# Performance work log

Measured on AMD Instinct MI355X. Metric: run time of the kernel, lower is better.

Reference implementation:

```python
import jax, jax.numpy as jnp
import numpy as np
from jax import lax

F_SIZE = 128
N_HEADS = 8
HEAD_D = F_SIZE // N_HEADS
LANE_F = 64
NUM_PREDS = 6


def _layernorm(x, g, b, eps=1e-5):
    m = x.mean(-1, keepdims=True)
    v = jnp.var(x, axis=-1, keepdims=True)
    return (x - m) * lax.rsqrt(v + eps) * g + b


def _lstm_cell(x, h, c, wih, whh, bih, bhh):
    # PyTorch LSTMCell: gates ordered i, f, g, o
    gates = x @ wih.T + bih + h @ whh.T + bhh
    i, f, g, o = jnp.split(gates, 4, axis=-1)
    c2 = jax.nn.sigmoid(f) * c + jax.nn.sigmoid(i) * jnp.tanh(g)
    h2 = jax.nn.sigmoid(o) * jnp.tanh(c2)
    return h2, c2


def _to_xy(dl, yaw):
    return jnp.concatenate([dl * jnp.cos(yaw), dl * jnp.sin(yaw)], axis=-1)


def _attention(tok_pos, h_ego, h, lane_tok, key_mask, wq, wk, wv, wo, pos_w, pos_b):
    # tokens = [ego, vehicles], keys/values = [tokens, lanes]
    B = h_ego.shape[0]
    tok = jnp.concatenate([h_ego, h], axis=1) + tok_pos @ pos_w + pos_b  # [B,N1,F]
    kv = jnp.concatenate([tok, lane_tok], axis=1)  # [B,N1+L,F]
    q = (tok @ wq).reshape(B, -1, N_HEADS, HEAD_D)
    k = (kv @ wk).reshape(B, -1, N_HEADS, HEAD_D)
    v = (kv @ wv).reshape(B, -1, N_HEADS, HEAD_D)
    s = jnp.einsum('bqhd,bkhd->bhqk', q, k) / jnp.asarray(np.sqrt(HEAD_D), jnp.float32)
    s = jnp.where(key_mask[:, None, None, :] > 0, s, -1e9)
    a = jax.nn.softmax(s, axis=-1)
    o = jnp.einsum('bhqk,bkhd->bqhd', a, v).reshape(B, -1, F_SIZE) @ wo
    tok = tok + o
    return tok[:, :1], tok[:, 1:]


def _forward(input, init_pos, lane_input, mask_input, lane_mask,
             conv_w, conv_b, pos_w, pos_b,
             lane_w1, lane_b1, lane_w2, lane_b2, lane_to_f,
             wq, wk, wv, wo, ln_ego_g, ln_ego_b, ln_g, ln_b,
             ego_wih, ego_whh, ego_bih, ego_bhh,
             veh_wih, veh_whh, veh_bih, veh_bhh,
             out_ego_w, out_ego_b, out_w, out_b, len_pred):
    T, B, N1, _ = input.shape
    V = N1 - 1
    Hh = T - 2  # valid conv over time with kernel 3

    # shared conv_input applied to ego+vehicles at once (same weights in original)
    x = jnp.transpose(input, (1, 3, 2, 0))  # [B,2,N1,T]
    feat = lax.conv_general_dilated(x, conv_w, (1, 1), 'VALID',
                                    dimension_numbers=('NCHW', 'OIHW', 'NCHW'))
    feat = feat + conv_b[None, :, None, None]
    feat = jnp.transpose(feat, (3, 0, 2, 1))  # [Hh,B,N1,F]
    h_ego_seq, h_seq = feat[:, :, :1], feat[:, :, 1:]

    # lane embedding: per-point MLP + mean pool
    lanes = jax.nn.relu(lane_input @ lane_w1 + lane_b1)
    lanes = jax.nn.relu(lanes @ lane_w2 + lane_b2).mean(axis=2)  # [B,L,LANE_F]
    lane_tok = lanes @ lane_to_f  # [B,L,F]
    key_mask = jnp.concatenate([mask_input, lane_mask], axis=1)  # [B,N1+L]

    pos0 = init_pos[0]
    pe0, pv0 = pos0[:, :1], pos0[:, 1:]

    def cell_step(hx_ego, cx_ego, hx, cx, he, hv, pe, pv):
        tok_pos = jnp.concatenate([pe, pv], axis=1)
        ae, av = _attention(tok_pos, he, hv, lane_tok, key_mask, wq, wk, wv, wo, pos_w, pos_b)
        ae = _layernorm(ae.reshape(B, F_SIZE), ln_ego_g, ln_ego_b)
        av = _layernorm(av.reshape(B * V, F_SIZE), ln_g, ln_b)
        hx_ego, cx_ego = _lstm_cell(ae, hx_ego, cx_ego, ego_wih, ego_whh, ego_bih, ego_bhh)
        hx, cx = _lstm_cell(av, hx, cx, veh_wih, veh_whh, veh_bih, veh_bhh)
        return hx_ego, cx_ego, hx, cx

    def hist_step(carry, xs):
        hx_ego, cx_ego, hx, cx, pe, pv = carry
        he, hv, xe, xv = xs
        pe = pe + _to_xy(xe[..., 0:1], xe[..., 1:2])
        pv = pv + _to_xy(xv[..., 0:1], xv[..., 1:2])
        hx_ego, cx_ego, hx, cx = cell_step(hx_ego, cx_ego, hx, cx, he, hv, pe, pv)
        return (hx_ego, cx_ego, hx, cx, pe, pv), None

    carry0 = (jnp.zeros((B, F_SIZE)), jnp.zeros((B, F_SIZE)),
              jnp.zeros((B * V, F_SIZE)), jnp.zeros((B * V, F_SIZE)), pe0, pv0)
    xs = (h_ego_seq, h_seq, input[:Hh, :, :1, :].transpose(0, 1, 2, 3), input[:Hh, :, 1:, :])
    carry, _ = lax.scan(hist_step, carry0, xs)
    hx_ego, cx_ego, hx, cx, pe, pv = carry

    pe = jnp.repeat(pe[:, :, None, :], NUM_PREDS, axis=2)  # [B,1,P,2]
    pv = jnp.repeat(pv[:, :, None, :], NUM_PREDS, axis=2)  # [B,V,P,2]

    def pred_step(carry, _):
        hx_ego, cx_ego, hx, cx, pe, pv = carry
        he = hx_ego.reshape(B, 1, F_SIZE)
        hv = hx.reshape(B, V, F_SIZE)
        hx_ego, cx_ego, hx, cx = cell_step(hx_ego, cx_ego, hx, cx, he, hv,
                                           pe.mean(axis=2), pv.mean(axis=2))
        oe = (hx_ego @ out_ego_w + out_ego_b).reshape(B, 1, NUM_PREDS, 6)
        ov = (hx @ out_w + out_b).reshape(B, V, NUM_PREDS, 6)
        pe = pe + _to_xy(oe[..., 0:1], oe[..., 1:2])
        pv = pv + _to_xy(ov[..., 0:1], ov[..., 1:2])
        y = jnp.concatenate([
            jnp.concatenate([pe, oe[..., 2:6]], axis=-1),
            jnp.concatenate([pv, ov[..., 2:6]], axis=-1)], axis=1)  # [B,N1,P,6]
        return (hx_ego, cx_ego, hx, cx, pe, pv), y

    carry = (hx_ego, cx_ego, hx, cx, pe, pv)
    _, ys = lax.scan(pred_step, carry, None, length=len_pred)
    return ys  # [len_pred,B,N1,NUM_PREDS,6]


def setup_inputs() -> dict:
    key = jax.random.key(0)
    ks = jax.random.split(key, 40)
    B, T, N1, L, PTS = 128, 22, 32, 64, 10
    F, LF, G4, P6 = F_SIZE, LANE_F, 4 * F_SIZE, NUM_PREDS * 6
    s = 0.05
    inp = {}
    inp['input'] = jax.random.normal(ks[0], (T, B, N1, 2), jnp.float32) * 0.1
    inp['init_pos'] = jax.random.normal(ks[1], (1, B, N1, 2), jnp.float32) * 10.0
    inp['lane_input'] = jax.random.normal(ks[2], (B, L, PTS, 2), jnp.float32)
    inp['mask_input'] = jnp.ones((B, N1), jnp.float32)
    inp['lane_mask'] = jnp.ones((B, L), jnp.float32)
    inp['conv_w'] = jax.random.normal(ks[3], (F, 2, 1, 3), jnp.float32) * s
    inp['conv_b'] = jnp.zeros((F,), jnp.float32)
    inp['pos_w'] = jax.random.normal(ks[4], (2, F), jnp.float32) * s
    inp['pos_b'] = jnp.zeros((F,), jnp.float32)
    inp['lane_w1'] = jax.random.normal(ks[5], (2, LF), jnp.float32) * s
    inp['lane_b1'] = jnp.zeros((LF,), jnp.float32)
    inp['lane_w2'] = jax.random.normal(ks[6], (LF, LF), jnp.float32) * s
    inp['lane_b2'] = jnp.zeros((LF,), jnp.float32)
    inp['lane_to_f'] = jax.random.normal(ks[7], (LF, F), jnp.float32) * s
    inp['wq'] = jax.random.normal(ks[8], (F, F), jnp.float32) * s
    inp['wk'] = jax.random.normal(ks[9], (F, F), jnp.float32) * s
    inp['wv'] = jax.random.normal(ks[10], (F, F), jnp.float32) * s
    inp['wo'] = jax.random.normal(ks[11], (F, F), jnp.float32) * s
    inp['ln_ego_g'] = jnp.ones((F,), jnp.float32)
    inp['ln_ego_b'] = jnp.zeros((F,), jnp.float32)
    inp['ln_g'] = jnp.ones((F,), jnp.float32)
    inp['ln_b'] = jnp.zeros((F,), jnp.float32)
    inp['ego_wih'] = jax.random.normal(ks[12], (G4, F), jnp.float32) * s
    inp['ego_whh'] = jax.random.normal(ks[13], (G4, F), jnp.float32) * s
    inp['ego_bih'] = jnp.zeros((G4,), jnp.float32)
    inp['ego_bhh'] = jnp.zeros((G4,), jnp.float32)
    inp['veh_wih'] = jax.random.normal(ks[14], (G4, F), jnp.float32) * s
    inp['veh_whh'] = jax.random.normal(ks[15], (G4, F), jnp.float32) * s
    inp['veh_bih'] = jnp.zeros((G4,), jnp.float32)
    inp['veh_bhh'] = jnp.zeros((G4,), jnp.float32)
    inp['out_ego_w'] = jax.random.normal(ks[16], (F, P6), jnp.float32) * s
    inp['out_ego_b'] = jnp.zeros((P6,), jnp.float32)
    inp['out_w'] = jax.random.normal(ks[17], (F, P6), jnp.float32) * s
    inp['out_b'] = jnp.zeros((P6,), jnp.float32)
    inp['len_pred'] = 30
    return inp


def reference(input, init_pos, lane_input, mask_input, lane_mask,
              conv_w, conv_b, pos_w, pos_b,
              lane_w1, lane_b1, lane_w2, lane_b2, lane_to_f,
              wq, wk, wv, wo, ln_ego_g, ln_ego_b, ln_g, ln_b,
              ego_wih, ego_whh, ego_bih, ego_bhh,
              veh_wih, veh_whh, veh_bih, veh_bhh,
              out_ego_w, out_ego_b, out_w, out_b, len_pred):
    return _forward(input, init_pos, lane_input, mask_input, lane_mask,
                    conv_w, conv_b, pos_w, pos_b,
                    lane_w1, lane_b1, lane_w2, lane_b2, lane_to_f,
                    wq, wk, wv, wo, ln_ego_g, ln_ego_b, ln_g, ln_b,
                    ego_wih, ego_whh, ego_bih, ego_bhh,
                    veh_wih, veh_whh, veh_bih, veh_bhh,
                    out_ego_w, out_ego_b, out_w, out_b, len_pred)
```

## Files before the change

### kernel.cpp

```cpp
#include <hip/hip_runtime.h>
#include <hip/hip_bf16.h>
#include <math.h>

constexpr int B   = 128;
constexpr int T   = 22;
constexpr int N1  = 32;
constexpr int HH  = 20;
constexpr int L   = 64;
constexpr int PTS = 10;
constexpr int F   = 128;
constexpr int LF  = 64;
constexpr int NH  = 8;
constexpr int HD  = 16;
constexpr int KVN = 96;
constexpr int G4  = 512;
constexpr int NP  = 6;
constexpr int P6  = 36;
constexpr int LEN = 30;

__device__ __forceinline__ float sigmoidf(float x) { return 1.f / (1.f + expf(-x)); }


__global__ void k_lane_tok(const float* __restrict__ lane_input,
                           const float* __restrict__ w1, const float* __restrict__ b1,
                           const float* __restrict__ w2, const float* __restrict__ b2,
                           const float* __restrict__ to_f,
                           float* __restrict__ kvbuf) {
    int bl = blockIdx.x; int b = bl / L, l = bl % L;
    int tid = threadIdx.x;
    __shared__ float h1[PTS][LF];
    __shared__ float m[LF];
    const float* xin = lane_input + ((size_t)(b * L + l) * PTS) * 2;
    float w10 = w1[tid], w11 = w1[LF + tid], bb1 = b1[tid];
    for (int p = 0; p < PTS; ++p) {
        float v = xin[p * 2] * w10 + xin[p * 2 + 1] * w11 + bb1;
        h1[p][tid] = fmaxf(v, 0.f);
    }
    __syncthreads();
    float acc = 0.f;
    for (int p = 0; p < PTS; ++p) {
        float s = b2[tid];
        for (int h = 0; h < LF; ++h) s += h1[p][h] * w2[h * LF + tid];
        acc += fmaxf(s, 0.f);
    }
    m[tid] = acc * (1.f / PTS);
    __syncthreads();
    float* out = kvbuf + ((size_t)(b * KVN) + 32 + l) * F;
    for (int f = tid; f < F; f += LF) {
        float s = 0.f;
        for (int j = 0; j < LF; ++j) s += m[j] * to_f[j * F + f];
        out[f] = s;
    }
}

__global__ void k_hist_pos(const float* __restrict__ input,
                           const float* __restrict__ init_pos,
                           float* __restrict__ hist_pos) {
    int idx = blockIdx.x * blockDim.x + threadIdx.x;
    if (idx >= B * N1) return;
    float px = init_pos[idx * 2], py = init_pos[idx * 2 + 1];
    int b = idx / N1, n = idx % N1;
    for (int t = 0; t < HH; ++t) {
        const float* ip = input + ((size_t)(t * B + b) * N1 + n) * 2;
        float dl = ip[0], yaw = ip[1];
        px += dl * cosf(yaw);
        py += dl * sinf(yaw);
        float* hp = hist_pos + ((size_t)(t * B + b) * N1 + n) * 2;
        hp[0] = px; hp[1] = py;
    }
}

__global__ void k_transpose_w(const float* __restrict__ w, float* __restrict__ wt) {
    int i = blockIdx.x * blockDim.x + threadIdx.x;
    if (i >= G4 * F) return;
    int j = i / F, k2 = i % F;
    wt[k2 * G4 + j] = w[i];
}

__global__ void k_init_predpos(const float* __restrict__ hist_pos, float* __restrict__ pred_pos) {
    int i = blockIdx.x * blockDim.x + threadIdx.x;
    if (i >= B * N1 * NP * 2) return;
    int c = i & 1;
    int bn = i / (2 * NP);
    pred_pos[i] = hist_pos[((size_t)(HH - 1) * B * N1 + bn) * 2 + c];
}


__global__ void k_tok_hist(const float* __restrict__ input,
                           const float* __restrict__ conv_w, const float* __restrict__ conv_b,
                           const float* __restrict__ pos_w, const float* __restrict__ pos_b,
                           const float* __restrict__ hist_pos,
                           float* __restrict__ kvbuf, int t) {
    int bn = blockIdx.x; int b = bn / N1, n = bn % N1;
    int f = threadIdx.x;
    float acc = conv_b[f];
#pragma unroll
    for (int kt = 0; kt < 3; ++kt) {
        const float* ip = input + ((size_t)((t + kt) * B + b) * N1 + n) * 2;
        acc += ip[0] * conv_w[(f * 2 + 0) * 3 + kt] + ip[1] * conv_w[(f * 2 + 1) * 3 + kt];
    }
    const float* hp = hist_pos + ((size_t)(t * B + b) * N1 + n) * 2;
    acc += hp[0] * pos_w[f] + hp[1] * pos_w[F + f] + pos_b[f];
    kvbuf[((size_t)b * KVN + n) * F + f] = acc;
}

__global__ void k_tok_pred(const float* __restrict__ h, const float* __restrict__ pred_pos,
                           const float* __restrict__ pos_w, const float* __restrict__ pos_b,
                           float* __restrict__ kvbuf) {
    int bn = blockIdx.x; int b = bn / N1, n = bn % N1;
    int f = threadIdx.x;
    const float* pp = pred_pos + (size_t)bn * NP * 2;
    float mx = 0.f, my = 0.f;
#pragma unroll
    for (int p = 0; p < NP; ++p) { mx += pp[p * 2]; my += pp[p * 2 + 1]; }
    mx *= (1.f / NP); my *= (1.f / NP);
    float tok = h[(size_t)bn * F + f] + mx * pos_w[f] + my * pos_w[F + f] + pos_b[f];
    kvbuf[((size_t)b * KVN + n) * F + f] = tok;
}

__global__ void k_qkv(const float* __restrict__ kvbuf,
                      const float* __restrict__ wq, const float* __restrict__ wk,
                      const float* __restrict__ wv,
                      float* __restrict__ qbuf, float* __restrict__ kbuf,
                      float* __restrict__ vbuf) {
    int g = blockIdx.x % 28, b = blockIdx.x / 28;
    int j = threadIdx.x;
    const float* W; float* out; int row0;
    if (g < 4)       { W = wq; row0 = g * 8;        out = qbuf + ((size_t)b * N1  + row0) * F; }
    else if (g < 16) { W = wk; row0 = (g - 4) * 8;  out = kbuf + ((size_t)b * KVN + row0) * F; }
    else             { W = wv; row0 = (g - 16) * 8; out = vbuf + ((size_t)b * KVN + row0) * F; }
    const float* in = kvbuf + ((size_t)b * KVN + row0) * F;
    __shared__ float rows[8][F];
#pragma unroll
    for (int r = 0; r < 8; ++r) rows[r][j] = in[r * F + j];
    __syncthreads();
    float acc[8] = {0, 0, 0, 0, 0, 0, 0, 0};
    for (int k2 = 0; k2 < F; ++k2) {
        float w = W[k2 * F + j];
#pragma unroll
        for (int r = 0; r < 8; ++r) acc[r] += rows[r][k2] * w;
    }
#pragma unroll
    for (int r = 0; r < 8; ++r) out[r * F + j] = acc[r];
}

__global__ void k_attn(const float* __restrict__ qbuf, const float* __restrict__ kbuf,
                       const float* __restrict__ vbuf,
                       const float* __restrict__ mask_in, const float* __restrict__ lane_mask,
                       float* __restrict__ attno) {
    int h = blockIdx.x % NH, b = blockIdx.x / NH;
    int tid = threadIdx.x;
    __shared__ float qs[N1][HD];
    __shared__ float s[N1][KVN];
    for (int i = tid; i < N1 * HD; i += 128) {
        int qr = i / HD, d = i % HD;
        qs[qr][d] = qbuf[((size_t)b * N1 + qr) * F + h * HD + d];
    }
    __syncthreads();
    for (int i = tid; i < N1 * KVN; i += 128) {
        int qr = i / KVN, kc = i % KVN;
        const float* kp = kbuf + ((size_t)b * KVN + kc) * F + h * HD;
        float acc = 0.f;
#pragma unroll
        for (int d = 0; d < HD; ++d) acc += qs[qr][d] * kp[d];
        float mval = (kc < N1) ? mask_in[b * N1 + kc] : lane_mask[b * L + (kc - N1)];
        s[qr][kc] = (mval > 0.f) ? acc * 0.25f : -1e9f;
    }
    __syncthreads();
    if (tid < N1) {
        float mx = -1e30f;
        for (int kc = 0; kc < KVN; ++kc) mx = fmaxf(mx, s[tid][kc]);
        float sum = 0.f;
        for (int kc = 0; kc < KVN; ++kc) { float e = expf(s[tid][kc] - mx); s[tid][kc] = e; sum += e; }
        float inv = 1.f / sum;
        for (int kc = 0; kc < KVN; ++kc) s[tid][kc] *= inv;
    }
    __syncthreads();
    for (int i = tid; i < N1 * HD; i += 128) {
        int qr = i / HD, d = i % HD;
        float acc = 0.f;
        for (int kc = 0; kc < KVN; ++kc)
            acc += s[qr][kc] * vbuf[((size_t)b * KVN + kc) * F + h * HD + d];
        attno[((size_t)b * N1 + qr) * F + h * HD + d] = acc;
    }
}

__global__ void k_proj_ln(const float* __restrict__ attno, const float* __restrict__ kvbuf,
                          const float* __restrict__ wo,
                          const float* __restrict__ ln_ego_g, const float* __restrict__ ln_ego_b,
                          const float* __restrict__ ln_g, const float* __restrict__ ln_b,
                          float* __restrict__ xln) {
    int gi = blockIdx.x; int b = gi / 8, n0 = (gi % 8) * 4;
    int j = threadIdx.x;
    __shared__ float arows[4][F];
    __shared__ float p1[2], p2[2];
#pragma unroll
    for (int r = 0; r < 4; ++r) arows[r][j] = attno[((size_t)b * N1 + n0 + r) * F + j];
    __syncthreads();
    float acc[4] = {0, 0, 0, 0};
    for (int k2 = 0; k2 < F; ++k2) {
        float w = wo[k2 * F + j];
#pragma unroll
        for (int r = 0; r < 4; ++r) acc[r] += arows[r][k2] * w;
    }
    for (int r = 0; r < 4; ++r) {
        int n = n0 + r;
        float x = kvbuf[((size_t)b * KVN + n) * F + j] + acc[r];
        float s1 = x, s2 = x * x;
#pragma unroll
        for (int off = 32; off > 0; off >>= 1) {
            s1 += __shfl_down(s1, off, 64);
            s2 += __shfl_down(s2, off, 64);
        }
        if ((j & 63) == 0) { p1[j >> 6] = s1; p2[j >> 6] = s2; }
        __syncthreads();
        float mean = (p1[0] + p1[1]) * (1.f / F);
        float var  = (p2[0] + p2[1]) * (1.f / F) - mean * mean;
        float rstd = rsqrtf(var + 1e-5f);
        const float* g  = (n == 0) ? ln_ego_g : ln_g;
        const float* bb = (n == 0) ? ln_ego_b : ln_b;
        xln[((size_t)b * N1 + n) * F + j] = (x - mean) * rstd * g[j] + bb[j];
        __syncthreads();
    }
}

__global__ void k_lstm(const float* __restrict__ xln,
                       const float* __restrict__ ego_wih_t, const float* __restrict__ ego_whh_t,
                       const float* __restrict__ ego_bih, const float* __restrict__ ego_bhh,
                       const float* __restrict__ veh_wih_t, const float* __restrict__ veh_whh_t,
                       const float* __restrict__ veh_bih, const float* __restrict__ veh_bhh,
                       float* __restrict__ h, float* __restrict__ c) {
    int n = blockIdx.x / 16; int b0 = (blockIdx.x % 16) * 8;
    int j = threadIdx.x;
    const float *wih, *whh, *bih, *bhh;
    if (n == 0) { wih = ego_wih_t; whh = ego_whh_t; bih = ego_bih; bhh = ego_bhh; }
    else        { wih = veh_wih_t; whh = veh_whh_t; bih = veh_bih; bhh = veh_bhh; }
    __shared__ float xr[8][F], hr[8][F];
    __shared__ float gs[8][G4];
    for (int i = j; i < 8 * F; i += 512) {
        int r = i / F, k2 = i % F;
        size_t bn = (size_t)(b0 + r) * N1 + n;
        xr[r][k2] = xln[bn * F + k2];
        hr[r][k2] = h[bn * F + k2];
    }
    __syncthreads();
    float acc[8];
    float bsum = bih[j] + bhh[j];
#pragma unroll
    for (int r = 0; r < 8; ++r) acc[r] = bsum;
    for (int k2 = 0; k2 < F; ++k2) {
        float w1 = wih[k2 * G4 + j];
        float w2 = whh[k2 * G4 + j];
#pragma unroll
        for (int r = 0; r < 8; ++r) acc[r] += xr[r][k2] * w1 + hr[r][k2] * w2;
    }
#pragma unroll
    for (int r = 0; r < 8; ++r) gs[r][j] = acc[r];
    __syncthreads();
    for (int i = j; i < 8 * F; i += 512) {
        int r = i / F, f = i % F;
        size_t bn = (size_t)(b0 + r) * N1 + n;
        float ig = gs[r][f], fg = gs[r][F + f], gg = gs[r][2 * F + f], og = gs[r][3 * F + f];
        float cold = c[bn * F + f];
        float c2 = sigmoidf(fg) * cold + sigmoidf(ig) * tanhf(gg);
        float h2 = sigmoidf(og) * tanhf(c2);
        c[bn * F + f] = c2;
        h[bn * F + f] = h2;
    }
}

__global__ void k_pred_out(const float* __restrict__ h,
                           const float* __restrict__ out_ego_w, const float* __restrict__ out_ego_b,
                           const float* __restrict__ out_w, const float* __restrict__ out_b,
                           float* __restrict__ pred_pos, float* __restrict__ out, int step) {
    int bn = blockIdx.x; int n = bn % N1;
    int j = threadIdx.x;
    __shared__ float hrow[F];
    __shared__ float o36[P6];
    hrow[j] = h[(size_t)bn * F + j];
    hrow[j + 64] = h[(size_t)bn * F + j + 64];
    __syncthreads();
    const float* W  = (n == 0) ? out_ego_w : out_w;
    const float* bb = (n == 0) ? out_ego_b : out_b;
    if (j < P6) {
        float acc = bb[j];
        for (int k2 = 0; k2 < F; ++k2) acc += hrow[k2] * W[k2 * P6 + j];
        o36[j] = acc;
    }
    __syncthreads();
    if (j < NP) {
        float dl = o36[j * 6], yaw = o36[j * 6 + 1];
        float* pp = pred_pos + ((size_t)bn * NP + j) * 2;
        float px = pp[0] + dl * cosf(yaw);
        float py = pp[1] + dl * sinf(yaw);
        pp[0] = px; pp[1] = py;
        float* y = out + (size_t)step * B * N1 * P6 + ((size_t)bn * NP + j) * 6;
        y[0] = px; y[1] = py;
        y[2] = o36[j * 6 + 2]; y[3] = o36[j * 6 + 3];
        y[4] = o36[j * 6 + 4]; y[5] = o36[j * 6 + 5];
    }
}

extern "C" void kernel_launch(void* const* d_in, const int* in_sizes, int n_in,
                              void* d_out, int out_size, void* d_ws, size_t ws_size,
                              hipStream_t stream) {
    const float* input      = (const float*)d_in[0];
    const float* init_pos   = (const float*)d_in[1];
    const float* lane_input = (const float*)d_in[2];
    const float* mask_input = (const float*)d_in[3];
    const float* lane_mask  = (const float*)d_in[4];
    const float* conv_w     = (const float*)d_in[5];
    const float* conv_b     = (const float*)d_in[6];
    const float* pos_w      = (const float*)d_in[7];
    const float* pos_b      = (const float*)d_in[8];
    const float* lane_w1    = (const float*)d_in[9];
    const float* lane_b1    = (const float*)d_in[10];
    const float* lane_w2    = (const float*)d_in[11];
    const float* lane_b2    = (const float*)d_in[12];
    const float* lane_to_f  = (const float*)d_in[13];
    const float* wq         = (const float*)d_in[14];
    const float* wk         = (const float*)d_in[15];
    const float* wv         = (const float*)d_in[16];
    const float* wo         = (const float*)d_in[17];
    const float* ln_ego_g   = (const float*)d_in[18];
    const float* ln_ego_b   = (const float*)d_in[19];
    const float* ln_g       = (const float*)d_in[20];
    const float* ln_b       = (const float*)d_in[21];
    const float* ego_wih    = (const float*)d_in[22];
    const float* ego_whh    = (const float*)d_in[23];
    const float* ego_bih    = (const float*)d_in[24];
    const float* ego_bhh    = (const float*)d_in[25];
    const float* veh_wih    = (const float*)d_in[26];
    const float* veh_whh    = (const float*)d_in[27];
    const float* veh_bih    = (const float*)d_in[28];
    const float* veh_bhh    = (const float*)d_in[29];
    const float* out_ego_w  = (const float*)d_in[30];
    const float* out_ego_b  = (const float*)d_in[31];
    const float* out_w      = (const float*)d_in[32];
    const float* out_b      = (const float*)d_in[33];

    float* out = (float*)d_out;
    float* ws = (float*)d_ws;

    float* kv       = ws;
    float* qb       = kv + (size_t)B * KVN * F;
    float* kb       = qb + (size_t)B * N1 * F;
    float* vb       = kb + (size_t)B * KVN * F;
    float* attno    = vb + (size_t)B * KVN * F;
    float* xln      = attno + (size_t)B * N1 * F;
    float* hbuf     = xln + (size_t)B * N1 * F;
    float* cbuf     = hbuf + (size_t)B * N1 * F;
    float* hist_pos = cbuf + (size_t)B * N1 * F;
    float* pred_pos = hist_pos + (size_t)HH * B * N1 * 2;
    float* wt       = pred_pos + (size_t)B * N1 * NP * 2;
    float* ego_wih_t = wt;
    float* ego_whh_t = wt + (size_t)G4 * F;
    float* veh_wih_t = wt + (size_t)2 * G4 * F;
    float* veh_whh_t = wt + (size_t)3 * G4 * F;

    hipMemsetAsync(hbuf, 0, (size_t)B * N1 * F * sizeof(float), stream);
    hipMemsetAsync(cbuf, 0, (size_t)B * N1 * F * sizeof(float), stream);
    k_lane_tok<<<B * L, 64, 0, stream>>>(lane_input, lane_w1, lane_b1, lane_w2, lane_b2,
                                         lane_to_f, kv);
    k_hist_pos<<<(B * N1 + 255) / 256, 256, 0, stream>>>(input, init_pos, hist_pos);
    k_transpose_w<<<(G4 * F + 255) / 256, 256, 0, stream>>>(ego_wih, ego_wih_t);
    k_transpose_w<<<(G4 * F + 255) / 256, 256, 0, stream>>>(ego_whh, ego_whh_t);
    k_transpose_w<<<(G4 * F + 255) / 256, 256, 0, stream>>>(veh_wih, veh_wih_t);
    k_transpose_w<<<(G4 * F + 255) / 256, 256, 0, stream>>>(veh_whh, veh_whh_t);

    for (int t = 0; t < HH; ++t) {
        k_tok_hist<<<B * N1, F, 0, stream>>>(input, conv_w, conv_b, pos_w, pos_b,
                                             hist_pos, kv, t);
        k_qkv<<<B * 28, F, 0, stream>>>(kv, wq, wk, wv, qb, kb, vb);
        k_attn<<<B * NH, 128, 0, stream>>>(qb, kb, vb, mask_input, lane_mask, attno);
        k_proj_ln<<<B * 8, 128, 0, stream>>>(attno, kv, wo, ln_ego_g, ln_ego_b, ln_g, ln_b, xln);
        k_lstm<<<N1 * 16, G4, 0, stream>>>(xln, ego_wih_t, ego_whh_t, ego_bih, ego_bhh,
                                           veh_wih_t, veh_whh_t, veh_bih, veh_bhh, hbuf, cbuf);
    }

    k_init_predpos<<<(B * N1 * NP * 2 + 255) / 256, 256, 0, stream>>>(hist_pos, pred_pos);

    for (int s = 0; s < LEN; ++s) {
        k_tok_pred<<<B * N1, F, 0, stream>>>(hbuf, pred_pos, pos_w, pos_b, kv);
        k_qkv<<<B * 28, F, 0, stream>>>(kv, wq, wk, wv, qb, kb, vb);
        k_attn<<<B * NH, 128, 0, stream>>>(qb, kb, vb, mask_input, lane_mask, attno);
        k_proj_ln<<<B * 8, 128, 0, stream>>>(attno, kv, wo, ln_ego_g, ln_ego_b, ln_g, ln_b, xln);
        k_lstm<<<N1 * 16, G4, 0, stream>>>(xln, ego_wih_t, ego_whh_t, ego_bih, ego_bhh,
                                           veh_wih_t, veh_whh_t, veh_bih, veh_bhh, hbuf, cbuf);
        k_pred_out<<<B * N1, 64, 0, stream>>>(hbuf, out_ego_w, out_ego_b, out_w, out_b,
                                              pred_pos, out, s);
    }
}
```

Baseline: 6.342 ms.

## Fuse per-step kernels and hoist loop-invariant lane K/V projection

Cuts the per-step kernel chain from five or six launches to three. Token building is fused with the Q/K/V projection, attention is fused with the output projection and LayerNorm (one block per batch), and the LSTM is fused with the prediction head. Lane K/V projections never change across steps, so they are computed once before the loops instead of every step. The trade-off is much less parallelism per launch: the attention kernel runs only 128 blocks and loops over heads serially, and the LSTM kernel runs 256 blocks with 16 rows each, which may underfill the GPU.

```diff
diff --git a/kernel.cpp b/kernel.cpp
--- a/kernel.cpp
+++ b/kernel.cpp
@@ -3,7 +3,6 @@
 #include <math.h>
 
 constexpr int B   = 128;
-constexpr int T   = 22;
 constexpr int N1  = 32;
 constexpr int HH  = 20;
 constexpr int L   = 64;
@@ -45,17 +44,49 @@
     }
     m[tid] = acc * (1.f / PTS);
     __syncthreads();
-    float* out = kvbuf + ((size_t)(b * KVN) + 32 + l) * F;
+    float* outp = kvbuf + ((size_t)(b * KVN) + 32 + l) * F;
     for (int f = tid; f < F; f += LF) {
         float s = 0.f;
         for (int j = 0; j < LF; ++j) s += m[j] * to_f[j * F + f];
-        out[f] = s;
+        outp[f] = s;
+    }
+}
+
+__global__ void k_lane_kv(const float* __restrict__ kvbuf,
+                          const float* __restrict__ wk, const float* __restrict__ wv,
+                          float* __restrict__ kb, float* __restrict__ vb) {
+    int g = blockIdx.x & 7, b = blockIdx.x >> 3;
+    int n0 = 32 + g * 8;
+    int tid = threadIdx.x;
+    int j = tid & 127, rh = tid >> 7;
+    __shared__ float tok[8][F];
+    for (int i = tid; i < 8 * F; i += 256) {
+        int r = i >> 7, c = i & 127;
+        tok[r][c] = kvbuf[((size_t)b * KVN + n0 + r) * F + c];
+    }
+    __syncthreads();
+    float ak[4] = {0, 0, 0, 0}, av[4] = {0, 0, 0, 0};
+    int r0 = rh * 4;
+    for (int k2 = 0; k2 < F; ++k2) {
+        float wkv = wk[k2 * F + j], wvv = wv[k2 * F + j];
+#pragma unroll
+        for (int r = 0; r < 4; ++r) {
+            float x = tok[r0 + r][k2];
+            ak[r] += x * wkv; av[r] += x * wvv;
+        }
+    }
+#pragma unroll
+    for (int r = 0; r < 4; ++r) {
+        int n = n0 + r0 + r;
+        kb[((size_t)b * KVN + n) * F + j] = ak[r];
+        vb[((size_t)b * KVN + n) * F + j] = av[r];
     }
 }
 
 __global__ void k_hist_pos(const float* __restrict__ input,
                            const float* __restrict__ init_pos,
-                           float* __restrict__ hist_pos) {
+                           float* __restrict__ hist_pos,
+                           float* __restrict__ pred_pos) {
     int idx = blockIdx.x * blockDim.x + threadIdx.x;
     if (idx >= B * N1) return;
     float px = init_pos[idx * 2], py = init_pos[idx * 2 + 1];
@@ -68,197 +99,209 @@
         float* hp = hist_pos + ((size_t)(t * B + b) * N1 + n) * 2;
         hp[0] = px; hp[1] = py;
     }
-}
-
-__global__ void k_transpose_w(const float* __restrict__ w, float* __restrict__ wt) {
+#pragma unroll
+    for (int p = 0; p < NP; ++p) {
+        pred_pos[((size_t)idx * NP + p) * 2 + 0] = px;
+        pred_pos[((size_t)idx * NP + p) * 2 + 1] = py;
+    }
+}
+
+__global__ void k_transpose_all(const float* __restrict__ w0, const float* __restrict__ w1,
+                                const float* __restrict__ w2, const float* __restrict__ w3,
+                                float* __restrict__ wt) {
     int i = blockIdx.x * blockDim.x + threadIdx.x;
-    if (i >= G4 * F) return;
-    int j = i / F, k2 = i % F;
-    wt[k2 * G4 + j] = w[i];
-}
-
-__global__ void k_init_predpos(const float* __restrict__ hist_pos, float* __restrict__ pred_pos) {
-    int i = blockIdx.x * blockDim.x + threadIdx.x;
-    if (i >= B * N1 * NP * 2) return;
-    int c = i & 1;
-    int bn = i / (2 * NP);
-    pred_pos[i] = hist_pos[((size_t)(HH - 1) * B * N1 + bn) * 2 + c];
-}
-
-
-__global__ void k_tok_hist(const float* __restrict__ input,
-                           const float* __restrict__ conv_w, const float* __restrict__ conv_b,
-                           const float* __restrict__ pos_w, const float* __restrict__ pos_b,
-                           const float* __restrict__ hist_pos,
-                           float* __restrict__ kvbuf, int t) {
-    int bn = blockIdx.x; int b = bn / N1, n = bn % N1;
-    int f = threadIdx.x;
-    float acc = conv_b[f];
-#pragma unroll
-    for (int kt = 0; kt < 3; ++kt) {
-        const float* ip = input + ((size_t)((t + kt) * B + b) * N1 + n) * 2;
-        acc += ip[0] * conv_w[(f * 2 + 0) * 3 + kt] + ip[1] * conv_w[(f * 2 + 1) * 3 + kt];
-    }
-    const float* hp = hist_pos + ((size_t)(t * B + b) * N1 + n) * 2;
-    acc += hp[0] * pos_w[f] + hp[1] * pos_w[F + f] + pos_b[f];
-    kvbuf[((size_t)b * KVN + n) * F + f] = acc;
-}
-
-__global__ void k_tok_pred(const float* __restrict__ h, const float* __restrict__ pred_pos,
-                           const float* __restrict__ pos_w, const float* __restrict__ pos_b,
-                           float* __restrict__ kvbuf) {
-    int bn = blockIdx.x; int b = bn / N1, n = bn % N1;
-    int f = threadIdx.x;
-    const float* pp = pred_pos + (size_t)bn * NP * 2;
-    float mx = 0.f, my = 0.f;
-#pragma unroll
-    for (int p = 0; p < NP; ++p) { mx += pp[p * 2]; my += pp[p * 2 + 1]; }
-    mx *= (1.f / NP); my *= (1.f / NP);
-    float tok = h[(size_t)bn * F + f] + mx * pos_w[f] + my * pos_w[F + f] + pos_b[f];
-    kvbuf[((size_t)b * KVN + n) * F + f] = tok;
-}
-
-__global__ void k_qkv(const float* __restrict__ kvbuf,
-                      const float* __restrict__ wq, const float* __restrict__ wk,
-                      const float* __restrict__ wv,
-                      float* __restrict__ qbuf, float* __restrict__ kbuf,
-                      float* __restrict__ vbuf) {
-    int g = blockIdx.x % 28, b = blockIdx.x / 28;
-    int j = threadIdx.x;
-    const float* W; float* out; int row0;
-    if (g < 4)       { W = wq; row0 = g * 8;        out = qbuf + ((size_t)b * N1  + row0) * F; }
-    else if (g < 16) { W = wk; row0 = (g - 4) * 8;  out = kbuf + ((size_t)b * KVN + row0) * F; }
-    else             { W = wv; row0 = (g - 16) * 8; out = vbuf + ((size_t)b * KVN + row0) * F; }
-    const float* in = kvbuf + ((size_t)b * KVN + row0) * F;
-    __shared__ float rows[8][F];
-#pragma unroll
-    for (int r = 0; r < 8; ++r) rows[r][j] = in[r * F + j];
-    __syncthreads();
+    if (i >= 4 * G4 * F) return;
+    int m = i / (G4 * F), rem = i % (G4 * F);
+    int j = rem / F, k2 = rem % F;
+    const float* src = (m == 0) ? w0 : (m == 1) ? w1 : (m == 2) ? w2 : w3;
+    wt[(size_t)m * G4 * F + (size_t)k2 * G4 + j] = src[rem];
+}
+
+
+__global__ void k_tok_qkv(const float* __restrict__ input, const float* __restrict__ hist_pos,
+                          const float* __restrict__ h, const float* __restrict__ pred_pos,
+                          const float* __restrict__ conv_w, const float* __restrict__ conv_b,
+                          const float* __restrict__ pos_w, const float* __restrict__ pos_b,
+                          const float* __restrict__ wq, const float* __restrict__ wk,
+                          const float* __restrict__ wv,
+                          float* __restrict__ kvbuf, float* __restrict__ qb,
+                          float* __restrict__ kb, float* __restrict__ vb,
+                          int mode, int t) {
+    int g = blockIdx.x & 3, b = blockIdx.x >> 2;
+    int n0 = g * 8;
+    int tid = threadIdx.x;
+    int j = tid & 127, rh = tid >> 7;
+    __shared__ float tok[8][F];
+    for (int i = tid; i < 8 * F; i += 256) {
+        int r = i >> 7, c = i & 127;
+        int n = n0 + r;
+        float acc;
+        if (mode == 0) {
+            acc = conv_b[c];
+#pragma unroll
+            for (int kt = 0; kt < 3; ++kt) {
+                const float* ip = input + ((size_t)((t + kt) * B + b) * N1 + n) * 2;
+                acc += ip[0] * conv_w[(c * 2 + 0) * 3 + kt] + ip[1] * conv_w[(c * 2 + 1) * 3 + kt];
+            }
+            const float* hp = hist_pos + ((size_t)(t * B + b) * N1 + n) * 2;
+            acc += hp[0] * pos_w[c] + hp[1] * pos_w[F + c] + pos_b[c];
+        } else {
+            const float* pp = pred_pos + ((size_t)(b * N1 + n)) * NP * 2;
+            float mx = 0.f, my = 0.f;
+#pragma unroll
+            for (int p = 0; p < NP; ++p) { mx += pp[p * 2]; my += pp[p * 2 + 1]; }
+            mx *= (1.f / NP); my *= (1.f / NP);
+            acc = h[((size_t)b * N1 + n) * F + c] + mx * pos_w[c] + my * pos_w[F + c] + pos_b[c];
+        }
+        tok[r][c] = acc;
+        kvbuf[((size_t)b * KVN + n) * F + c] = acc;
+    }
+    __syncthreads();
+    float aq[4] = {0, 0, 0, 0}, ak[4] = {0, 0, 0, 0}, av[4] = {0, 0, 0, 0};
+    int r0 = rh * 4;
+    for (int k2 = 0; k2 < F; ++k2) {
+        float wqv = wq[k2 * F + j], wkv = wk[k2 * F + j], wvv = wv[k2 * F + j];
+#pragma unroll
+        for (int r = 0; r < 4; ++r) {
+            float x = tok[r0 + r][k2];
+            aq[r] += x * wqv; ak[r] += x * wkv; av[r] += x * wvv;
+        }
+    }
+#pragma unroll
+    for (int r = 0; r < 4; ++r) {
+        int n = n0 + r0 + r;
+        qb[((size_t)b * N1 + n) * F + j]  = aq[r];
+        kb[((size_t)b * KVN + n) * F + j] = ak[r];
+        vb[((size_t)b * KVN + n) * F + j] = av[r];
+    }
+}
+
+__global__ void k_attn_proj_ln(const float* __restrict__ qb, const float* __restrict__ kb,
+                               const float* __restrict__ vb, const float* __restrict__ kvbuf,
+                               const float* __restrict__ mask_in, const float* __restrict__ lane_mask,
+                               const float* __restrict__ wo,
+                               const float* __restrict__ ln_ego_g, const float* __restrict__ ln_ego_b,
+                               const float* __restrict__ ln_g, const float* __restrict__ ln_b,
+                               float* __restrict__ xln) {
+    int b = blockIdx.x;
+    int tid = threadIdx.x;
+    __shared__ float qh[N1][HD];
+    __shared__ float kh[KVN][HD];
+    __shared__ float vh[KVN][HD];
+    __shared__ float sc[N1][KVN + 1];
+    __shared__ float ao[N1][F];
+    __shared__ float xb[N1][F];
+    __shared__ float red[N1][2];
+
+    for (int h = 0; h < NH; ++h) {
+        if (tid < N1 * HD) {
+            int qr = tid >> 4, d = tid & 15;
+            qh[qr][d] = qb[((size_t)b * N1 + qr) * F + h * HD + d];
+        }
+        for (int i = tid; i < KVN * HD; i += 512) {
+            int kc = i >> 4, d = i & 15;
+            kh[kc][d] = kb[((size_t)b * KVN + kc) * F + h * HD + d];
+            vh[kc][d] = vb[((size_t)b * KVN + kc) * F + h * HD + d];
+        }
+        __syncthreads();
+        for (int i = tid; i < N1 * KVN; i += 512) {
+            int qr = i / KVN, kc = i % KVN;
+            float acc = 0.f;
+#pragma unroll
+            for (int d = 0; d < HD; ++d) acc += qh[qr][d] * kh[kc][d];
+            float mval = (kc < N1) ? mask_in[b * N1 + kc] : lane_mask[b * L + (kc - N1)];
+            sc[qr][kc] = (mval > 0.f) ? acc * 0.25f : -1e9f;
+        }
+        __syncthreads();
+        if (tid < N1) {
+            float mx = -1e30f;
+            for (int kc = 0; kc < KVN; ++kc) mx = fmaxf(mx, sc[tid][kc]);
+            float sum = 0.f;
+            for (int kc = 0; kc < KVN; ++kc) { float e = expf(sc[tid][kc] - mx); sc[tid][kc] = e; sum += e; }
+            float inv = 1.f / sum;
+            for (int kc = 0; kc < KVN; ++kc) sc[tid][kc] *= inv;
+        }
+        __syncthreads();
+        if (tid < N1 * HD) {
+            int qr = tid >> 4, d = tid & 15;
+            float acc = 0.f;
+            for (int kc = 0; kc < KVN; ++kc) acc += sc[qr][kc] * vh[kc][d];
+            ao[qr][h * HD + d] = acc;
+        }
+        __syncthreads();
+    }
+    int j = tid & 127, rh = tid >> 7;
     float acc[8] = {0, 0, 0, 0, 0, 0, 0, 0};
-    for (int k2 = 0; k2 < F; ++k2) {
-        float w = W[k2 * F + j];
-#pragma unroll
-        for (int r = 0; r < 8; ++r) acc[r] += rows[r][k2] * w;
-    }
-#pragma unroll
-    for (int r = 0; r < 8; ++r) out[r * F + j] = acc[r];
-}
-
-__global__ void k_attn(const float* __restrict__ qbuf, const float* __restrict__ kbuf,
-                       const float* __restrict__ vbuf,
-                       const float* __restrict__ mask_in, const float* __restrict__ lane_mask,
-                       float* __restrict__ attno) {
-    int h = blockIdx.x % NH, b = blockIdx.x / NH;
-    int tid = threadIdx.x;
-    __shared__ float qs[N1][HD];
-    __shared__ float s[N1][KVN];
-    for (int i = tid; i < N1 * HD; i += 128) {
-        int qr = i / HD, d = i % HD;
-        qs[qr][d] = qbuf[((size_t)b * N1 + qr) * F + h * HD + d];
-    }
-    __syncthreads();
-    for (int i = tid; i < N1 * KVN; i += 128) {
-        int qr = i / KVN, kc = i % KVN;
-        const float* kp = kbuf + ((size_t)b * KVN + kc) * F + h * HD;
-        float acc = 0.f;
-#pragma unroll
-        for (int d = 0; d < HD; ++d) acc += qs[qr][d] * kp[d];
-        float mval = (kc < N1) ? mask_in[b * N1 + kc] : lane_mask[b * L + (kc - N1)];
-        s[qr][kc] = (mval > 0.f) ? acc * 0.25f : -1e9f;
-    }
-    __syncthreads();
-    if (tid < N1) {
-        float mx = -1e30f;
-        for (int kc = 0; kc < KVN; ++kc) mx = fmaxf(mx, s[tid][kc]);
-        float sum = 0.f;
-        for (int kc = 0; kc < KVN; ++kc) { float e = expf(s[tid][kc] - mx); s[tid][kc] = e; sum += e; }
-        float inv = 1.f / sum;
-        for (int kc = 0; kc < KVN; ++kc) s[tid][kc] *= inv;
-    }
-    __syncthreads();
-    for (int i = tid; i < N1 * HD; i += 128) {
-        int qr = i / HD, d = i % HD;
-        float acc = 0.f;
-        for (int kc = 0; kc < KVN; ++kc)
-            acc += s[qr][kc] * vbuf[((size_t)b * KVN + kc) * F + h * HD + d];
-        attno[((size_t)b * N1 + qr) * F + h * HD + d] = acc;
-    }
-}
-
-__global__ void k_proj_ln(const float* __restrict__ attno, const float* __restrict__ kvbuf,
-                          const float* __restrict__ wo,
-                          const float* __restrict__ ln_ego_g, const float* __restrict__ ln_ego_b,
-                          const float* __restrict__ ln_g, const float* __restrict__ ln_b,
-                          float* __restrict__ xln) {
-    int gi = blockIdx.x; int b = gi / 8, n0 = (gi % 8) * 4;
-    int j = threadIdx.x;
-    __shared__ float arows[4][F];
-    __shared__ float p1[2], p2[2];
-#pragma unroll
-    for (int r = 0; r < 4; ++r) arows[r][j] = attno[((size_t)b * N1 + n0 + r) * F + j];
-    __syncthreads();
-    float acc[4] = {0, 0, 0, 0};
+    int r0 = rh * 8;
     for (int k2 = 0; k2 < F; ++k2) {
         float w = wo[k2 * F + j];
 #pragma unroll
-        for (int r = 0; r < 4; ++r) acc[r] += arows[r][k2] * w;
-    }
-    for (int r = 0; r < 4; ++r) {
-        int n = n0 + r;
-        float x = kvbuf[((size_t)b * KVN + n) * F + j] + acc[r];
-        float s1 = x, s2 = x * x;
-#pragma unroll
-        for (int off = 32; off > 0; off >>= 1) {
-            s1 += __shfl_down(s1, off, 64);
-            s2 += __shfl_down(s2, off, 64);
-        }
-        if ((j & 63) == 0) { p1[j >> 6] = s1; p2[j >> 6] = s2; }
-        __syncthreads();
-        float mean = (p1[0] + p1[1]) * (1.f / F);
-        float var  = (p2[0] + p2[1]) * (1.f / F) - mean * mean;
-        float rstd = rsqrtf(var + 1e-5f);
-        const float* g  = (n == 0) ? ln_ego_g : ln_g;
-        const float* bb = (n == 0) ? ln_ego_b : ln_b;
-        xln[((size_t)b * N1 + n) * F + j] = (x - mean) * rstd * g[j] + bb[j];
-        __syncthreads();
-    }
-}
-
-__global__ void k_lstm(const float* __restrict__ xln,
-                       const float* __restrict__ ego_wih_t, const float* __restrict__ ego_whh_t,
-                       const float* __restrict__ ego_bih, const float* __restrict__ ego_bhh,
-                       const float* __restrict__ veh_wih_t, const float* __restrict__ veh_whh_t,
-                       const float* __restrict__ veh_bih, const float* __restrict__ veh_bhh,
-                       float* __restrict__ h, float* __restrict__ c) {
-    int n = blockIdx.x / 16; int b0 = (blockIdx.x % 16) * 8;
+        for (int r = 0; r < 8; ++r) acc[r] += ao[r0 + r][k2] * w;
+    }
+#pragma unroll
+    for (int r = 0; r < 8; ++r) {
+        int n = r0 + r;
+        xb[n][j] = kvbuf[((size_t)b * KVN + n) * F + j] + acc[r];
+    }
+    __syncthreads();
+    if (tid < N1) {
+        float s1 = 0.f, s2 = 0.f;
+        for (int c = 0; c < F; ++c) { float x = xb[tid][c]; s1 += x; s2 += x * x; }
+        float mean = s1 * (1.f / F);
+        float var = s2 * (1.f / F) - mean * mean;
+        red[tid][0] = mean;
+        red[tid][1] = rsqrtf(var + 1e-5f);
+    }
+    __syncthreads();
+    for (int i = tid; i < N1 * F; i += 512) {
+        int r = i >> 7, c = i & 127;
+        const float* g  = (r == 0) ? ln_ego_g : ln_g;
+        const float* bb = (r == 0) ? ln_ego_b : ln_b;
+        xln[((size_t)b * N1 + r) * F + c] = (xb[r][c] - red[r][0]) * red[r][1] * g[c] + bb[c];
+    }
+}
+
+__global__ void k_lstm_pred(const float* __restrict__ xln,
+                            const float* __restrict__ ego_wih_t, const float* __restrict__ ego_whh_t,
+                            const float* __restrict__ ego_bih, const float* __restrict__ ego_bhh,
+                            const float* __restrict__ veh_wih_t, const float* __restrict__ veh_whh_t,
+                            const float* __restrict__ veh_bih, const float* __restrict__ veh_bhh,
+                            float* __restrict__ h, float* __restrict__ c,
+                            const float* __restrict__ out_ego_w, const float* __restrict__ out_ego_b,
+                            const float* __restrict__ out_w, const float* __restrict__ out_b,
+                            float* __restrict__ pred_pos, float* __restrict__ out,
+                            int mode, int step) {
+    int n = blockIdx.x >> 3, bg = blockIdx.x & 7;
+    int b0 = bg * 16;
     int j = threadIdx.x;
     const float *wih, *whh, *bih, *bhh;
     if (n == 0) { wih = ego_wih_t; whh = ego_whh_t; bih = ego_bih; bhh = ego_bhh; }
     else        { wih = veh_wih_t; whh = veh_whh_t; bih = veh_bih; bhh = veh_bhh; }
-    __shared__ float xr[8][F], hr[8][F];
-    __shared__ float gs[8][G4];
-    for (int i = j; i < 8 * F; i += 512) {
-        int r = i / F, k2 = i % F;
+    __shared__ float xr[16][F];
+    __shared__ float hr2[16][F];
+    __shared__ float gs[16][G4];
+    for (int i = j; i < 16 * F; i += 512) {
+        int r = i >> 7, k2 = i & 127;
         size_t bn = (size_t)(b0 + r) * N1 + n;
-        xr[r][k2] = xln[bn * F + k2];
-        hr[r][k2] = h[bn * F + k2];
-    }
-    __syncthreads();
-    float acc[8];
+        xr[r][k2]  = xln[bn * F + k2];
+        hr2[r][k2] = h[bn * F + k2];
+    }
+    __syncthreads();
+    float acc[16];
     float bsum = bih[j] + bhh[j];
 #pragma unroll
-    for (int r = 0; r < 8; ++r) acc[r] = bsum;
+    for (int r = 0; r < 16; ++r) acc[r] = bsum;
     for (int k2 = 0; k2 < F; ++k2) {
-        float w1 = wih[k2 * G4 + j];
-        float w2 = whh[k2 * G4 + j];
-#pragma unroll
-        for (int r = 0; r < 8; ++r) acc[r] += xr[r][k2] * w1 + hr[r][k2] * w2;
-    }
-#pragma unroll
-    for (int r = 0; r < 8; ++r) gs[r][j] = acc[r];
-    __syncthreads();
-    for (int i = j; i < 8 * F; i += 512) {
-        int r = i / F, f = i % F;
+        float w1 = wih[(size_t)k2 * G4 + j];
+        float w2 = whh[(size_t)k2 * G4 + j];
+#pragma unroll
+        for (int r = 0; r < 16; ++r) acc[r] += xr[r][k2] * w1 + hr2[r][k2] * w2;
+    }
+#pragma unroll
+    for (int r = 0; r < 16; ++r) gs[r][j] = acc[r];
+    __syncthreads();
+    for (int i = j; i < 16 * F; i += 512) {
+        int r = i >> 7, f = i & 127;
         size_t bn = (size_t)(b0 + r) * N1 + n;
         float ig = gs[r][f], fg = gs[r][F + f], gg = gs[r][2 * F + f], og = gs[r][3 * F + f];
         float cold = c[bn * F + f];
@@ -266,38 +309,32 @@
         float h2 = sigmoidf(og) * tanhf(c2);
         c[bn * F + f] = c2;
         h[bn * F + f] = h2;
-    }
-}
-
-__global__ void k_pred_out(const float* __restrict__ h,
-                           const float* __restrict__ out_ego_w, const float* __restrict__ out_ego_b,
-                           const float* __restrict__ out_w, const float* __restrict__ out_b,
-                           float* __restrict__ pred_pos, float* __restrict__ out, int step) {
-    int bn = blockIdx.x; int n = bn % N1;
-    int j = threadIdx.x;
-    __shared__ float hrow[F];
-    __shared__ float o36[P6];
-    hrow[j] = h[(size_t)bn * F + j];
-    hrow[j + 64] = h[(size_t)bn * F + j + 64];
-    __syncthreads();
-    const float* W  = (n == 0) ? out_ego_w : out_w;
-    const float* bb = (n == 0) ? out_ego_b : out_b;
-    if (j < P6) {
-        float acc = bb[j];
-        for (int k2 = 0; k2 < F; ++k2) acc += hrow[k2] * W[k2 * P6 + j];
-        o36[j] = acc;
-    }
-    __syncthreads();
-    if (j < NP) {
-        float dl = o36[j * 6], yaw = o36[j * 6 + 1];
-        float* pp = pred_pos + ((size_t)bn * NP + j) * 2;
-        float px = pp[0] + dl * cosf(yaw);
-        float py = pp[1] + dl * sinf(yaw);
-        pp[0] = px; pp[1] = py;
-        float* y = out + (size_t)step * B * N1 * P6 + ((size_t)bn * NP + j) * 6;
-        y[0] = px; y[1] = py;
-        y[2] = o36[j * 6 + 2]; y[3] = o36[j * 6 + 3];
-        y[4] = o36[j * 6 + 4]; y[5] = o36[j * 6 + 5];
+        xr[r][f] = h2;
+    }
+    if (mode == 1) {
+        const float* W  = (n == 0) ? out_ego_w : out_w;
+        const float* bb = (n == 0) ? out_ego_b : out_b;
+        __syncthreads();
+        for (int i = j; i < 16 * P6; i += 512) {
+            int r = i / P6, jj = i % P6;
+            float a = bb[jj];
+            for (int k2 = 0; k2 < F; ++k2) a += xr[r][k2] * W[k2 * P6 + jj];
+            gs[r][jj] = a;
+        }
+        __syncthreads();
+        if (j < 16 * NP) {
+            int r = j / NP, p = j % NP;
+            size_t bn = (size_t)(b0 + r) * N1 + n;
+            float dl = gs[r][p * 6 + 0], yaw = gs[r][p * 6 + 1];
+            float* pp = pred_pos + (bn * NP + p) * 2;
+            float px = pp[0] + dl * cosf(yaw);
+            float py = pp[1] + dl * sinf(yaw);
+            pp[0] = px; pp[1] = py;
+            float* y = out + (size_t)step * B * N1 * P6 + (bn * NP + p) * 6;
+            y[0] = px; y[1] = py;
+            y[2] = gs[r][p * 6 + 2]; y[3] = gs[r][p * 6 + 3];
+            y[4] = gs[r][p * 6 + 4]; y[5] = gs[r][p * 6 + 5];
+        }
     }
 }
 
@@ -346,8 +383,7 @@
     float* qb       = kv + (size_t)B * KVN * F;
     float* kb       = qb + (size_t)B * N1 * F;
     float* vb       = kb + (size_t)B * KVN * F;
-    float* attno    = vb + (size_t)B * KVN * F;
-    float* xln      = attno + (size_t)B * N1 * F;
+    float* xln      = vb + (size_t)B * KVN * F;
     float* hbuf     = xln + (size_t)B * N1 * F;
     float* cbuf     = hbuf + (size_t)B * N1 * F;
     float* hist_pos = cbuf + (size_t)B * N1 * F;
@@ -362,32 +398,32 @@
     hipMemsetAsync(cbuf, 0, (size_t)B * N1 * F * sizeof(float), stream);
     k_lane_tok<<<B * L, 64, 0, stream>>>(lane_input, lane_w1, lane_b1, lane_w2, lane_b2,
                                          lane_to_f, kv);
-    k_hist_pos<<<(B * N1 + 255) / 256, 256, 0, stream>>>(input, init_pos, hist_pos);
-    k_transpose_w<<<(G4 * F + 255) / 256, 256, 0, stream>>>(ego_wih, ego_wih_t);
-    k_transpose_w<<<(G4 * F + 255) / 256, 256, 0, stream>>>(ego_whh, ego_whh_t);
-    k_transpose_w<<<(G4 * F + 255) / 256, 256, 0, stream>>>(veh_wih, veh_wih_t);
-    k_transpose_w<<<(G4 * F + 255) / 256, 256, 0, stream>>>(veh_whh, veh_whh_t);
+    k_hist_pos<<<(B * N1 + 255) / 256, 256, 0, stream>>>(input, init_pos, hist_pos, pred_pos);
+    k_transpose_all<<<(4 * G4 * F + 255) / 256, 256, 0, stream>>>(ego_wih, ego_whh, veh_wih,
+                                                                  veh_whh, wt);
+    k_lane_kv<<<B * 8, 256, 0, stream>>>(kv, wk, wv, kb, vb);
 
     for (int t = 0; t < HH; ++t) {
-        k_tok_hist<<<B * N1, F, 0, stream>>>(input, conv_w, conv_b, pos_w, pos_b,
-                                             hist_pos, kv, t);
-        k_qkv<<<B * 28, F, 0, stream>>>(kv, wq, wk, wv, qb, kb, vb);
-        k_attn<<<B * NH, 128, 0, stream>>>(qb, kb, vb, mask_input, lane_mask, attno);
-        k_proj_ln<<<B * 8, 128, 0, stream>>>(attno, kv, wo, ln_ego_g, ln_ego_b, ln_g, ln_b, xln);
-        k_lstm<<<N1 * 16, G4, 0, stream>>>(xln, ego_wih_t, ego_whh_t, ego_bih, ego_bhh,
-                                           veh_wih_t, veh_whh_t, veh_bih, veh_bhh, hbuf, cbuf);
-    }
-
-    k_init_predpos<<<(B * N1 * NP * 2 + 255) / 256, 256, 0, stream>>>(hist_pos, pred_pos);
+        k_tok_qkv<<<B * 4, 256, 0, stream>>>(input, hist_pos, hbuf, pred_pos,
+                                             conv_w, conv_b, pos_w, pos_b,
+                                             wq, wk, wv, kv, qb, kb, vb, 0, t);
+        k_attn_proj_ln<<<B, 512, 0, stream>>>(qb, kb, vb, kv, mask_input, lane_mask, wo,
+                                              ln_ego_g, ln_ego_b, ln_g, ln_b, xln);
+        k_lstm_pred<<<N1 * 8, 512, 0, stream>>>(xln, ego_wih_t, ego_whh_t, ego_bih, ego_bhh,
+                                                veh_wih_t, veh_whh_t, veh_bih, veh_bhh,
+                                                hbuf, cbuf, out_ego_w, out_ego_b, out_w, out_b,
+                                                pred_pos, out, 0, 0);
+    }
 
     for (int s = 0; s < LEN; ++s) {
-        k_tok_pred<<<B * N1, F, 0, stream>>>(hbuf, pred_pos, pos_w, pos_b, kv);
-        k_qkv<<<B * 28, F, 0, stream>>>(kv, wq, wk, wv, qb, kb, vb);
-        k_attn<<<B * NH, 128, 0, stream>>>(qb, kb, vb, mask_input, lane_mask, attno);
-        k_proj_ln<<<B * 8, 128, 0, stream>>>(attno, kv, wo, ln_ego_g, ln_ego_b, ln_g, ln_b, xln);
-        k_lstm<<<N1 * 16, G4, 0, stream>>>(xln, ego_wih_t, ego_whh_t, ego_bih, ego_bhh,
-                                           veh_wih_t, veh_whh_t, veh_bih, veh_bhh, hbuf, cbuf);
-        k_pred_out<<<B * N1, 64, 0, stream>>>(hbuf, out_ego_w, out_ego_b, out_w, out_b,
-                                              pred_pos, out, s);
-    }
-}
+        k_tok_qkv<<<B * 4, 256, 0, stream>>>(input, hist_pos, hbuf, pred_pos,
+                                             conv_w, conv_b, pos_w, pos_b,
+                                             wq, wk, wv, kv, qb, kb, vb, 1, 0);
+        k_attn_proj_ln<<<B, 512, 0, stream>>>(qb, kb, vb, kv, mask_input, lane_mask, wo,
+                                              ln_ego_g, ln_ego_b, ln_g, ln_b, xln);
+        k_lstm_pred<<<N1 * 8, 512, 0, stream>>>(xln, ego_wih_t, ego_whh_t, ego_bih, ego_bhh,
+                                                veh_wih_t, veh_whh_t, veh_bih, veh_bhh,
+                                                hbuf, cbuf, out_ego_w, out_ego_b, out_w, out_b,
+                                                pred_pos, out, 1, s);
+    }
+}
```

New measurement: 8.986 ms. +41.7%, slower.
